# Kernel tuning notes

Measured on AMD Instinct MI355X. Metric: run time of the kernel, lower is better.

Reference implementation:

```python
import jax, jax.numpy as jnp
import numpy as np

EMBED_DIM = 384
NUM_HEADS = 6
HEAD_DIM = EMBED_DIM // NUM_HEADS
SCALE = HEAD_DIM ** (-0.5)


def setup_inputs() -> dict:
    key = jax.random.key(0)
    ks = jax.random.split(key, 5)
    B, N, D = 8, 2048, EMBED_DIM
    x = jax.random.normal(ks[0], (B, N, D), dtype=jnp.float32)
    # Linear params, torch convention: weight [out, in], bias [out]
    w_qkv = jax.random.normal(ks[1], (3 * D, D), dtype=jnp.float32) * (D ** -0.5)
    b_qkv = jax.random.normal(ks[2], (3 * D,), dtype=jnp.float32) * 0.01
    w_out = jax.random.normal(ks[3], (D, D), dtype=jnp.float32) * (D ** -0.5)
    b_out = jax.random.normal(ks[4], (D,), dtype=jnp.float32) * 0.01
    return {"x": x, "w_qkv": w_qkv, "b_qkv": b_qkv, "w_out": w_out, "b_out": b_out}


def reference(x, w_qkv, b_qkv, w_out, b_out):
    B, N, D = x.shape
    H, Dh = NUM_HEADS, HEAD_DIM
    # qkv projection: [B,N,3D]
    qkv = jnp.einsum('bnd,ed->bne', x, w_qkv) + b_qkv
    qkv = qkv.reshape(B, N, 3, H, Dh).transpose(2, 0, 3, 1, 4)  # [3,B,H,N,Dh]
    q, k, v = qkv[0], qkv[1], qkv[2]
    # full NxN attention scores (faithful to original eager math)
    scores = jnp.einsum('bhnd,bhmd->bhnm', q, k) * SCALE  # [B,H,N,N]
    attn = jax.nn.softmax(scores, axis=-1)
    out = jnp.einsum('bhnm,bhmd->bhnd', attn, v)  # [B,H,N,Dh]
    out = out.transpose(0, 2, 1, 3).reshape(B, N, D)
    out = jnp.einsum('bnd,ed->bne', out, w_out) + b_out
    return out
```

## Files before the change

kernel.cpp:

```cpp
#include <hip/hip_runtime.h>

typedef unsigned short u16;
typedef unsigned int u32;
typedef float f32x4 __attribute__((ext_vector_type(4)));
typedef __bf16 bf16x8 __attribute__((ext_vector_type(8)));
typedef unsigned short u16x8 __attribute__((ext_vector_type(8)));
typedef unsigned short u16x4 __attribute__((ext_vector_type(4)));

__device__ inline u16 f2bf(float f) {
    return __builtin_bit_cast(u16, (__bf16)f);
}

__device__ inline void gll16(const u16* g, u16* l) {
    u16* gnc = const_cast<u16*>(g);
    __builtin_amdgcn_global_load_lds((__attribute__((address_space(1))) u32*)gnc,
                                     (__attribute__((address_space(3))) u32*)l,
                                     16, 0, 0);
}

#define MFMA(a, b, c) __builtin_amdgcn_mfma_f32_16x16x32_bf16((a), (b), (c), 0, 0, 0)

#define C_SHIFT 17.3123405f
#define Q_SCALE 0.1803368801f

__global__ __launch_bounds__(256)
void cvt_kernel(const float* __restrict__ X, const float* __restrict__ Wq,
                const float* __restrict__ Wo, u16* __restrict__ Xb,
                u16* __restrict__ Wqb, u16* __restrict__ Wob)
{
    int i = blockIdx.x * 256 + threadIdx.x;
    const float* src; u16* dst; int off;
    if (i < 1572864)       { src = X;  dst = Xb;  off = i; }
    else if (i < 1683456)  { src = Wq; dst = Wqb; off = i - 1572864; }
    else                   { src = Wo; dst = Wob; off = i - 1683456; }
    f32x4 v = *(const f32x4*)&src[off * 4];
    u16x4 p;
    for (int k = 0; k < 4; ++k) p[k] = f2bf(v[k]);
    *(u16x4*)&dst[off * 4] = p;
}

__global__ __launch_bounds__(256)
void qkv_kernel(const u16* __restrict__ Xb, const u16* __restrict__ Wqb,
                const float* __restrict__ B, u16* __restrict__ Qo,
                u16* __restrict__ Ko, u16* __restrict__ VTo)
{
    __shared__ __align__(128) u16 As[128][64];
    __shared__ __align__(128) u16 Ws[128][64];
    const int tid = threadIdx.x;
    const int m0 = blockIdx.x * 128;
    const int n0 = blockIdx.y * 128;
    const int wv = tid >> 6, lane = tid & 63;
    const int l15 = lane & 15, quad = lane >> 4;
    const int mw = (wv & 1) * 64, nw = (wv >> 1) * 64;

    const int lr = lane >> 3;
    const int gsrc = (lane & 7) ^ lr;
    const int swz = (quad ^ (l15 & 7)) * 8;

    f32x4 acc[4][4] = {};
    for (int kt = 0; kt < 384; kt += 64) {
        __syncthreads();
#pragma unroll
        for (int i = 0; i < 4; ++i) {
            int r = (wv * 4 + i) * 8 + lr;
            gll16(&Xb[(m0 + r) * 384 + kt + gsrc * 8], &As[(wv * 4 + i) * 8][0]);
            gll16(&Wqb[(n0 + r) * 384 + kt + gsrc * 8], &Ws[(wv * 4 + i) * 8][0]);
        }
        __syncthreads();
#pragma unroll
        for (int kc = 0; kc < 2; ++kc) {
            bf16x8 a[4], bf[4];
#pragma unroll
            for (int mi = 0; mi < 4; ++mi)
                a[mi] = *(const bf16x8*)&As[mw + mi * 16 + l15][swz ^ (kc << 5)];
#pragma unroll
            for (int nj = 0; nj < 4; ++nj)
                bf[nj] = *(const bf16x8*)&Ws[nw + nj * 16 + l15][swz ^ (kc << 5)];
#pragma unroll
            for (int mi = 0; mi < 4; ++mi)
#pragma unroll
                for (int nj = 0; nj < 4; ++nj)
                    acc[mi][nj] = MFMA(a[mi], bf[nj], acc[mi][nj]);
        }
    }
    for (int nj = 0; nj < 4; ++nj) {
        int col = n0 + nw + nj * 16 + l15;
        int t = col / 384;
        int h = (col % 384) / 64, dh = col & 63;
        float bias = B[col];
        for (int mi = 0; mi < 4; ++mi)
            for (int r = 0; r < 4; ++r) {
                int gm = m0 + mw + mi * 16 + quad * 4 + r;
                int bb = gm >> 11, n = gm & 2047;
                int bh = bb * 6 + h;
                float v = acc[mi][nj][r] + bias;
                if (t == 0)      Qo[(bh * 2048 + n) * 64 + dh] = f2bf(v * Q_SCALE);
                else if (t == 1) Ko[(bh * 2048 + n) * 64 + dh] = f2bf(v);
                else             VTo[(bh * 64 + dh) * 2048 + n] = f2bf(v);
            }
    }
}

__global__ __launch_bounds__(256)
void attn_kernel(const u16* __restrict__ Q, const u16* __restrict__ K,
                 const u16* __restrict__ VT, u16* __restrict__ O)
{
    __shared__ __align__(128) u16 Ks[2][64][64];
    __shared__ __align__(128) u16 VTs[2][64][64];
    __shared__ __align__(16) u16 Pbuf[128][72];

    const int tid = threadIdx.x;
    const int lin = blockIdx.y * 16 + blockIdx.x;
    const int lin2 = (lin & 7) * 96 + (lin >> 3);
    const int bh = lin2 >> 4;
    const int q0 = (lin2 & 15) * 128;
    const int wv = tid >> 6, lane = tid & 63;
    const int l15 = lane & 15, quad = lane >> 4;

    bf16x8 qf[2][2];
#pragma unroll
    for (int qb = 0; qb < 2; ++qb) {
        const u16* qptr = &Q[(bh * 2048 + q0 + wv * 32 + qb * 16 + l15) * 64 + quad * 8];
        qf[qb][0] = *(const bf16x8*)qptr;
        qf[qb][1] = *(const bf16x8*)(qptr + 32);
    }

    const int lr = lane >> 3;
    const int gsrc = (lane & 7) ^ lr;
    const u16* ksrc[2]; const u16* vsrc[2];
#pragma unroll
    for (int i = 0; i < 2; ++i) {
        int r = (wv * 2 + i) * 8 + lr;
        ksrc[i] = &K[(bh * 2048 + r) * 64 + gsrc * 8];
        vsrc[i] = &VT[(bh * 64 + r) * 2048 + gsrc * 8];
    }
    const int swz = (quad ^ (l15 & 7)) * 8;

    const f32x4 cinit = {-C_SHIFT, -C_SHIFT, -C_SHIFT, -C_SHIFT};
    float l_part[2] = {};
    f32x4 acc[2][4] = {};

#pragma unroll
    for (int i = 0; i < 2; ++i) {
        gll16(ksrc[i], &Ks[0][(wv * 2 + i) * 8][0]);
        gll16(vsrc[i], &VTs[0][(wv * 2 + i) * 8][0]);
    }

    for (int j = 0; j < 32; ++j) {
        const int cur = j & 1;
        __syncthreads();
        if (j < 31) {
#pragma unroll
            for (int i = 0; i < 2; ++i) {
                gll16(ksrc[i] + (j + 1) * 4096, &Ks[cur ^ 1][(wv * 2 + i) * 8][0]);
                gll16(vsrc[i] + (j + 1) * 64, &VTs[cur ^ 1][(wv * 2 + i) * 8][0]);
            }
        }

#pragma unroll
        for (int ct = 0; ct < 4; ++ct) {
            const u16* krow = &Ks[cur][ct * 16 + l15][0];
            bf16x8 a0 = *(const bf16x8*)(krow + swz);
            bf16x8 a1 = *(const bf16x8*)(krow + (swz ^ 32));
#pragma unroll
            for (int qb = 0; qb < 2; ++qb) {
                f32x4 s = MFMA(a0, qf[qb][0], cinit);
                s = MFMA(a1, qf[qb][1], s);
                u16x4 pk;
#pragma unroll
                for (int r = 0; r < 4; ++r) {
                    float p = __builtin_amdgcn_exp2f(s[r]);
                    l_part[qb] += p;
                    pk[r] = f2bf(p);
                }
                *(u16x4*)&Pbuf[wv * 32 + qb * 16 + l15][ct * 16 + quad * 4] = pk;
            }
        }

        bf16x8 pf[2][2];
#pragma unroll
        for (int qb = 0; qb < 2; ++qb) {
            const u16* pp = &Pbuf[wv * 32 + qb * 16 + l15][quad * 8];
            pf[qb][0] = *(const bf16x8*)pp;
            pf[qb][1] = *(const bf16x8*)(pp + 32);
        }
#pragma unroll
        for (int ct = 0; ct < 4; ++ct) {
            const u16* vrow = &VTs[cur][ct * 16 + l15][0];
            bf16x8 b0 = *(const bf16x8*)(vrow + swz);
            bf16x8 b1 = *(const bf16x8*)(vrow + (swz ^ 32));
#pragma unroll
            for (int qb = 0; qb < 2; ++qb) {
                acc[qb][ct] = MFMA(pf[qb][0], b0, acc[qb][ct]);
                acc[qb][ct] = MFMA(pf[qb][1], b1, acc[qb][ct]);
            }
        }
    }

    int b = bh / 6, h = bh % 6;
    for (int qb = 0; qb < 2; ++qb) {
        float lr2 = l_part[qb];
        lr2 += __shfl_xor(lr2, 16);
        lr2 += __shfl_xor(lr2, 32);
        float li[4];
        for (int r = 0; r < 4; ++r) li[r] = 1.0f / __shfl(lr2, quad * 4 + r);
        for (int ct = 0; ct < 4; ++ct)
            for (int r = 0; r < 4; ++r) {
                int row = q0 + wv * 32 + qb * 16 + quad * 4 + r;
                int dh = ct * 16 + l15;
                O[(b * 2048 + row) * 384 + h * 64 + dh] = f2bf(acc[qb][ct][r] * li[r]);
            }
    }
}

__global__ __launch_bounds__(256)
void outproj_kernel(const u16* __restrict__ A, const u16* __restrict__ Wob,
                    const float* __restrict__ B, float* __restrict__ out)
{
    __shared__ __align__(16) u16 As[64][72];
    __shared__ __align__(16) u16 Ws[64][72];
    const int tid = threadIdx.x;
    const int m0 = blockIdx.x * 64;
    const int n0 = blockIdx.y * 64;
    const int wv = tid >> 6, lane = tid & 63;
    const int l15 = lane & 15, quad = lane >> 4;

    f32x4 acc[4] = {};
    for (int kt = 0; kt < 384; kt += 64) {
        __syncthreads();
        for (int c = tid; c < 512; c += 256) {
            int row = c >> 3, cc = (c & 7) * 8;
            *(u16x8*)&As[row][cc] = *(const u16x8*)&A[(m0 + row) * 384 + kt + cc];
            *(u16x8*)&Ws[row][cc] = *(const u16x8*)&Wob[(n0 + row) * 384 + kt + cc];
        }
        __syncthreads();
        for (int kc = 0; kc < 2; ++kc) {
            bf16x8 b = *(const bf16x8*)&Ws[wv * 16 + l15][kc * 32 + quad * 8];
            for (int mi = 0; mi < 4; ++mi) {
                bf16x8 a = *(const bf16x8*)&As[mi * 16 + l15][kc * 32 + quad * 8];
                acc[mi] = MFMA(a, b, acc[mi]);
            }
        }
    }
    const int col = n0 + wv * 16 + l15;
    const float bias = B[col];
    for (int mi = 0; mi < 4; ++mi)
        for (int r = 0; r < 4; ++r) {
            int gm = m0 + mi * 16 + quad * 4 + r;
            out[gm * 384 + col] = acc[mi][r] + bias;
        }
}

extern "C" void kernel_launch(void* const* d_in, const int* in_sizes, int n_in,
                              void* d_out, int out_size, void* d_ws, size_t ws_size,
                              hipStream_t stream) {
    const float* x     = (const float*)d_in[0];
    const float* w_qkv = (const float*)d_in[1];
    const float* b_qkv = (const float*)d_in[2];
    const float* w_out = (const float*)d_in[3];
    const float* b_out = (const float*)d_in[4];
    float* out = (float*)d_out;

    char* ws = (char*)d_ws;
    u16* Qw   = (u16*)(ws);
    u16* Kw   = (u16*)(ws + 12582912);
    u16* VTw  = (u16*)(ws + 25165824);
    u16* XbAw = (u16*)(ws + 37748736);
    u16* Wqb  = (u16*)(ws + 50331648);
    u16* Wob  = (u16*)(ws + 51216384);

    cvt_kernel<<<6720, 256, 0, stream>>>(x, w_qkv, w_out, XbAw, Wqb, Wob);
    qkv_kernel<<<dim3(128, 9), 256, 0, stream>>>(XbAw, Wqb, b_qkv, Qw, Kw, VTw);
    attn_kernel<<<dim3(16, 48), 256, 0, stream>>>(Qw, Kw, VTw, XbAw);
    outproj_kernel<<<dim3(256, 6), 256, 0, stream>>>(XbAw, Wob, b_out, out);
}
```

Baseline: 203.6 us.

## Split attention key tiles across two wave groups with LDS reduction

Doubles the attention block to 512 threads. Each query-row group is now handled by two waves, each taking half of every 64-key tile, so per-wave MFMA work per iteration is halved. At the end, partial output accumulators and row sums are combined through shared memory, reusing the K/V and P buffers. This raises the number of waves per CU to hide latency, at the cost of an extra cross-wave reduction and two more barriers.

```diff
diff --git a/kernel.cpp b/kernel.cpp
--- a/kernel.cpp
+++ b/kernel.cpp
@@ -101,7 +101,7 @@
     }
 }
 
-__global__ __launch_bounds__(256)
+__global__ __launch_bounds__(512)
 void attn_kernel(const u16* __restrict__ Q, const u16* __restrict__ K,
                  const u16* __restrict__ VT, u16* __restrict__ O)
 {
@@ -116,50 +116,40 @@
     const int q0 = (lin2 & 15) * 128;
     const int wv = tid >> 6, lane = tid & 63;
     const int l15 = lane & 15, quad = lane >> 4;
+    const int qsub = wv & 3, kh = wv >> 2;
 
     bf16x8 qf[2][2];
 #pragma unroll
     for (int qb = 0; qb < 2; ++qb) {
-        const u16* qptr = &Q[(bh * 2048 + q0 + wv * 32 + qb * 16 + l15) * 64 + quad * 8];
+        const u16* qptr = &Q[(bh * 2048 + q0 + qsub * 32 + qb * 16 + l15) * 64 + quad * 8];
         qf[qb][0] = *(const bf16x8*)qptr;
         qf[qb][1] = *(const bf16x8*)(qptr + 32);
     }
 
     const int lr = lane >> 3;
     const int gsrc = (lane & 7) ^ lr;
-    const u16* ksrc[2]; const u16* vsrc[2];
-#pragma unroll
-    for (int i = 0; i < 2; ++i) {
-        int r = (wv * 2 + i) * 8 + lr;
-        ksrc[i] = &K[(bh * 2048 + r) * 64 + gsrc * 8];
-        vsrc[i] = &VT[(bh * 64 + r) * 2048 + gsrc * 8];
-    }
+    const u16* ksrc = &K[(bh * 2048 + wv * 8 + lr) * 64 + gsrc * 8];
+    const u16* vsrc = &VT[(bh * 64 + wv * 8 + lr) * 2048 + gsrc * 8];
     const int swz = (quad ^ (l15 & 7)) * 8;
 
     const f32x4 cinit = {-C_SHIFT, -C_SHIFT, -C_SHIFT, -C_SHIFT};
     float l_part[2] = {};
     f32x4 acc[2][4] = {};
 
-#pragma unroll
-    for (int i = 0; i < 2; ++i) {
-        gll16(ksrc[i], &Ks[0][(wv * 2 + i) * 8][0]);
-        gll16(vsrc[i], &VTs[0][(wv * 2 + i) * 8][0]);
-    }
+    gll16(ksrc, &Ks[0][wv * 8][0]);
+    gll16(vsrc, &VTs[0][wv * 8][0]);
 
     for (int j = 0; j < 32; ++j) {
         const int cur = j & 1;
         __syncthreads();
         if (j < 31) {
-#pragma unroll
-            for (int i = 0; i < 2; ++i) {
-                gll16(ksrc[i] + (j + 1) * 4096, &Ks[cur ^ 1][(wv * 2 + i) * 8][0]);
-                gll16(vsrc[i] + (j + 1) * 64, &VTs[cur ^ 1][(wv * 2 + i) * 8][0]);
-            }
-        }
-
-#pragma unroll
-        for (int ct = 0; ct < 4; ++ct) {
-            const u16* krow = &Ks[cur][ct * 16 + l15][0];
+            gll16(ksrc + (j + 1) * 4096, &Ks[cur ^ 1][wv * 8][0]);
+            gll16(vsrc + (j + 1) * 64, &VTs[cur ^ 1][wv * 8][0]);
+        }
+
+#pragma unroll
+        for (int c = 0; c < 2; ++c) {
+            const u16* krow = &Ks[cur][kh * 32 + c * 16 + l15][0];
             bf16x8 a0 = *(const bf16x8*)(krow + swz);
             bf16x8 a1 = *(const bf16x8*)(krow + (swz ^ 32));
 #pragma unroll
@@ -173,43 +163,67 @@
                     l_part[qb] += p;
                     pk[r] = f2bf(p);
                 }
-                *(u16x4*)&Pbuf[wv * 32 + qb * 16 + l15][ct * 16 + quad * 4] = pk;
+                *(u16x4*)&Pbuf[qsub * 32 + qb * 16 + l15][kh * 32 + c * 16 + quad * 4] = pk;
             }
         }
 
-        bf16x8 pf[2][2];
+        bf16x8 pf[2];
+#pragma unroll
+        for (int qb = 0; qb < 2; ++qb)
+            pf[qb] = *(const bf16x8*)&Pbuf[qsub * 32 + qb * 16 + l15][kh * 32 + quad * 8];
+#pragma unroll
+        for (int ct = 0; ct < 4; ++ct) {
+            bf16x8 bv = *(const bf16x8*)(&VTs[cur][ct * 16 + l15][0] + (swz ^ (kh << 5)));
+#pragma unroll
+            for (int qb = 0; qb < 2; ++qb)
+                acc[qb][ct] = MFMA(pf[qb], bv, acc[qb][ct]);
+        }
+    }
+
+    float lh[2];
+#pragma unroll
+    for (int qb = 0; qb < 2; ++qb) {
+        float t = l_part[qb];
+        t += __shfl_xor(t, 16);
+        t += __shfl_xor(t, 32);
+        lh[qb] = t;
+    }
+    __syncthreads();
+    float* lb = (float*)&Pbuf[0][0];
+    if (kh == 1) {
+        float* sb = (qsub < 2) ? (float*)&Ks[qsub][0][0] : (float*)&VTs[qsub - 2][0][0];
+#pragma unroll
+        for (int qb = 0; qb < 2; ++qb)
+#pragma unroll
+            for (int ct = 0; ct < 4; ++ct)
+                *(f32x4*)&sb[((qb * 4 + ct) * 64 + lane) * 4] = acc[qb][ct];
+        if (quad == 0) {
+            lb[qsub * 32 + l15] = lh[0];
+            lb[qsub * 32 + 16 + l15] = lh[1];
+        }
+    }
+    __syncthreads();
+    if (kh == 0) {
+        float* sb = (qsub < 2) ? (float*)&Ks[qsub][0][0] : (float*)&VTs[qsub - 2][0][0];
+#pragma unroll
+        for (int qb = 0; qb < 2; ++qb)
+#pragma unroll
+            for (int ct = 0; ct < 4; ++ct)
+                acc[qb][ct] += *(const f32x4*)&sb[((qb * 4 + ct) * 64 + lane) * 4];
+        lh[0] += lb[qsub * 32 + l15];
+        lh[1] += lb[qsub * 32 + 16 + l15];
+        int b = bh / 6, h = bh % 6;
 #pragma unroll
         for (int qb = 0; qb < 2; ++qb) {
-            const u16* pp = &Pbuf[wv * 32 + qb * 16 + l15][quad * 8];
-            pf[qb][0] = *(const bf16x8*)pp;
-            pf[qb][1] = *(const bf16x8*)(pp + 32);
-        }
-#pragma unroll
-        for (int ct = 0; ct < 4; ++ct) {
-            const u16* vrow = &VTs[cur][ct * 16 + l15][0];
-            bf16x8 b0 = *(const bf16x8*)(vrow + swz);
-            bf16x8 b1 = *(const bf16x8*)(vrow + (swz ^ 32));
-#pragma unroll
-            for (int qb = 0; qb < 2; ++qb) {
-                acc[qb][ct] = MFMA(pf[qb][0], b0, acc[qb][ct]);
-                acc[qb][ct] = MFMA(pf[qb][1], b1, acc[qb][ct]);
-            }
-        }
-    }
-
-    int b = bh / 6, h = bh % 6;
-    for (int qb = 0; qb < 2; ++qb) {
-        float lr2 = l_part[qb];
-        lr2 += __shfl_xor(lr2, 16);
-        lr2 += __shfl_xor(lr2, 32);
-        float li[4];
-        for (int r = 0; r < 4; ++r) li[r] = 1.0f / __shfl(lr2, quad * 4 + r);
-        for (int ct = 0; ct < 4; ++ct)
-            for (int r = 0; r < 4; ++r) {
-                int row = q0 + wv * 32 + qb * 16 + quad * 4 + r;
-                int dh = ct * 16 + l15;
-                O[(b * 2048 + row) * 384 + h * 64 + dh] = f2bf(acc[qb][ct][r] * li[r]);
-            }
+            float li[4];
+            for (int r = 0; r < 4; ++r) li[r] = 1.0f / __shfl(lh[qb], quad * 4 + r);
+            for (int ct = 0; ct < 4; ++ct)
+                for (int r = 0; r < 4; ++r) {
+                    int row = q0 + qsub * 32 + qb * 16 + quad * 4 + r;
+                    int dh = ct * 16 + l15;
+                    O[(b * 2048 + row) * 384 + h * 64 + dh] = f2bf(acc[qb][ct][r] * li[r]);
+                }
+        }
     }
 }
 
@@ -271,6 +285,6 @@
 
     cvt_kernel<<<6720, 256, 0, stream>>>(x, w_qkv, w_out, XbAw, Wqb, Wob);
     qkv_kernel<<<dim3(128, 9), 256, 0, stream>>>(XbAw, Wqb, b_qkv, Qw, Kw, VTw);
-    attn_kernel<<<dim3(16, 48), 256, 0, stream>>>(Qw, Kw, VTw, XbAw);
+    attn_kernel<<<dim3(16, 48), 512, 0, stream>>>(Qw, Kw, VTw, XbAw);
     outproj_kernel<<<dim3(256, 6), 256, 0, stream>>>(XbAw, Wob, b_out, out);
 }
```

Result: no change. 204.2 us (+0.3%).
